# Performance work log

Hardware: AMD Instinct MI355X
Metric: run time of the kernel (lower is better)

Reference implementation:

```python
import jax, jax.numpy as jnp
import numpy as np

HIDDEN_DIM = 256
Z_DIM = 64
B = 8
SRC_LEN = 2048
NUM_DIRS = 2


def setup_inputs() -> dict:
    key = jax.random.key(0)
    ks = jax.random.split(key, 7)
    return {
        "encoder_hidden_state": jax.random.normal(ks[0], (NUM_DIRS, B, HIDDEN_DIM), dtype=jnp.float32),
        "decoder_hidden_state": jax.random.normal(ks[1], (B, HIDDEN_DIM), dtype=jnp.float32),
        "latent_z_seq": jax.random.normal(ks[2], (B, SRC_LEN, Z_DIM), dtype=jnp.float32),
        "mask": jax.random.randint(ks[3], (B, SRC_LEN), 0, 2, dtype=jnp.int32),
        "weight_q": jax.random.normal(ks[4], (HIDDEN_DIM + Z_DIM, HIDDEN_DIM), dtype=jnp.float32),
        "weight_k": jax.random.normal(ks[5], (HIDDEN_DIM + Z_DIM, HIDDEN_DIM), dtype=jnp.float32),
        "weight_v": jax.random.normal(ks[6], (HIDDEN_DIM + Z_DIM, HIDDEN_DIM), dtype=jnp.float32),
    }


def reference(encoder_hidden_state, decoder_hidden_state, latent_z_seq, mask,
              weight_q, weight_k, weight_v):
    # decoder_hidden_state is accepted but unused (as in the original forward).
    src_len = latent_z_seq.shape[1]
    temperature = jnp.asarray(HIDDEN_DIM ** 0.5, latent_z_seq.dtype)
    # sum over directions/layers: [D,B,H] -> [B,H], broadcast along seq
    enc = jnp.sum(encoder_hidden_state, axis=0)  # [B,H]
    enc = jnp.broadcast_to(enc[:, None, :], (enc.shape[0], src_len, enc.shape[1]))
    attn_input = jnp.concatenate((enc, latent_z_seq), axis=2)  # [B,S,H+Z]
    q = jnp.einsum('bsd,dh->bsh', attn_input, weight_q)
    k = jnp.einsum('bsd,dh->bsh', attn_input, weight_k)
    v = jnp.einsum('bsd,dh->bsh', attn_input, weight_v)
    scores = jnp.einsum('bqh,bkh->bqk', q, k) / temperature  # [B,S,S]
    # mask[:, :, None] broadcasts along the key axis (masks query rows)
    scores = jnp.where(mask[:, :, None] == 0, jnp.asarray(-1e9, scores.dtype), scores)
    attn = jax.nn.softmax(scores, axis=-1)
    output = jnp.einsum('bqk,bkh->bqh', attn, v)  # [B,S,H]
    return (output, attn)
```

## Files before the change

### kernel.cpp

```cpp
#include <hip/hip_runtime.h>
#include <hip/hip_bf16.h>

#define B_ 8
#define S_ 2048
#define H_ 256
#define Z_ 64
#define CHK 32
#define NQCH 16
#define BS (B_*S_)

typedef short bf16x8 __attribute__((ext_vector_type(8)));
typedef float f32x4 __attribute__((ext_vector_type(4)));

__device__ __forceinline__ unsigned short f2bf(float f) {
  __hip_bfloat16 h = __float2bfloat16(f);
  return *reinterpret_cast<unsigned short*>(&h);
}
__device__ __forceinline__ float bf2f(unsigned short u) {
  __hip_bfloat16 h;
  *reinterpret_cast<unsigned short*>(&h) = u;
  return __bfloat162float(h);
}
__device__ __forceinline__ unsigned int pack2(float a, float b) {
  return (unsigned int)f2bf(a) | ((unsigned int)f2bf(b) << 16);
}

__device__ __forceinline__ void gl_lds16(const void* g, void* l) {
  __builtin_amdgcn_global_load_lds(
      (const __attribute__((address_space(1))) unsigned int*)(uintptr_t)g,
      (__attribute__((address_space(3))) unsigned int*)(uintptr_t)l,
      16, 0, 0);
}

__global__ __launch_bounds__(256) void k0_base(
    const float* __restrict__ enc, const float* __restrict__ Wq,
    const float* __restrict__ Wk, const float* __restrict__ Wv,
    float* __restrict__ q0, float* __restrict__ k0, float* __restrict__ v0) {
  int b = blockIdx.x;
  int h = threadIdx.x;
  __shared__ float encs[H_];
  encs[h] = enc[b*H_ + h] + enc[B_*H_ + b*H_ + h];
  __syncthreads();
  float aq = 0.f, ak = 0.f, av = 0.f;
  #pragma unroll 4
  for (int d = 0; d < H_; d++) {
    float e = encs[d];
    aq = fmaf(e, Wq[d*H_ + h], aq);
    ak = fmaf(e, Wk[d*H_ + h], ak);
    av = fmaf(e, Wv[d*H_ + h], av);
  }
  q0[b*H_ + h] = aq;
  k0[b*H_ + h] = ak;
  v0[b*H_ + h] = av;
}

__global__ __launch_bounds__(256) void k1_prep(
    const float* __restrict__ z, const float* __restrict__ Wq,
    const float* __restrict__ Wk, const float* __restrict__ Wv,
    const float* __restrict__ q0, const float* __restrict__ k0b, const float* __restrict__ v0,
    unsigned short* __restrict__ Qhi, unsigned short* __restrict__ Qlo,
    unsigned short* __restrict__ Khi, unsigned short* __restrict__ Klo,
    unsigned short* __restrict__ Vt) {
  int b  = blockIdx.x >> 7;
  int st = blockIdx.x & 127;
  int tid = threadIdx.x;
  __shared__ float zs[16*Z_];
  __shared__ float vbuf[16][H_];
  {
    const float4* zp = reinterpret_cast<const float4*>(z + ((size_t)b*S_ + st*16)*Z_);
    reinterpret_cast<float4*>(zs)[tid] = zp[tid];
  }
  __syncthreads();
  float bq = q0[b*H_ + tid], bk = k0b[b*H_ + tid], bv = v0[b*H_ + tid];
  float accq[16], acck[16], accv[16];
  #pragma unroll
  for (int s = 0; s < 16; s++) { accq[s] = bq; acck[s] = bk; accv[s] = bv; }
  #pragma unroll 2
  for (int z0 = 0; z0 < Z_; z0 += 8) {
    float wq[8], wk[8], wv[8];
    #pragma unroll
    for (int j = 0; j < 8; j++) {
      wq[j] = Wq[(H_+z0+j)*H_ + tid];
      wk[j] = Wk[(H_+z0+j)*H_ + tid];
      wv[j] = Wv[(H_+z0+j)*H_ + tid];
    }
    #pragma unroll
    for (int j = 0; j < 8; j++) {
      #pragma unroll
      for (int s = 0; s < 16; s++) {
        float zz = zs[s*Z_ + z0 + j];
        accq[s] = fmaf(zz, wq[j], accq[s]);
        acck[s] = fmaf(zz, wk[j], acck[s]);
        accv[s] = fmaf(zz, wv[j], accv[s]);
      }
    }
  }
  #pragma unroll
  for (int s = 0; s < 16; s++) {
    size_t row = ((size_t)b*S_ + st*16 + s)*H_ + tid;
    unsigned short qh = f2bf(accq[s]);
    Qhi[row] = qh;
    Qlo[row] = f2bf(accq[s] - bf2f(qh));
    unsigned short kh = f2bf(acck[s]);
    Khi[row] = kh;
    Klo[row] = f2bf(acck[s] - bf2f(kh));
    vbuf[s][tid] = accv[s];
  }
  __syncthreads();
  unsigned int pk[8];
  #pragma unroll
  for (int j = 0; j < 8; j++)
    pk[j] = pack2(vbuf[2*j][tid], vbuf[2*j+1][tid]);
  uint4* vt4 = reinterpret_cast<uint4*>(Vt + ((size_t)b*H_ + tid)*S_ + st*16);
  vt4[0] = make_uint4(pk[0], pk[1], pk[2], pk[3]);
  vt4[1] = make_uint4(pk[4], pk[5], pk[6], pk[7]);
}

__global__ __launch_bounds__(256, 2) void k2_flash(
    const unsigned short* __restrict__ Qhi, const unsigned short* __restrict__ Qlo,
    const unsigned short* __restrict__ Khi, const unsigned short* __restrict__ Klo,
    const int* __restrict__ mask,
    float* __restrict__ attn, float* __restrict__ Mq) {
  int bb    = blockIdx.x;
  int b     = bb & 7;
  int strip = (bb >> 3) & 15;
  int kq    = bb >> 7;
  int qb    = strip*128;
  int k0q   = kq*512;
  int tid  = threadIdx.x;
  int wave = tid >> 6;
  int lane = tid & 63;
  int l15  = lane & 15;
  int quad = lane >> 4;
  int qw   = qb + wave*32;

  __shared__ __align__(16) unsigned short KhiL[2][32*256];
  __shared__ __align__(16) unsigned short KloL[2][32*256];

  const unsigned short* KhiB = Khi + (size_t)b*S_*H_;
  const unsigned short* KloB = Klo + (size_t)b*S_*H_;

  int sub = lane >> 5;
  int c5  = lane & 31;

  auto dma_chunk = [&](int c) {
    int buf = c & 1;
    int kc = k0q + c*CHK;
    #pragma unroll
    for (int t = 0; t < 4; t++) {
      int i = wave*4 + t;
      int row = i*2 + sub;
      int lslot = c5 ^ ((row & 15) << 1);
      size_t gs = (size_t)(kc + row)*H_ + lslot*8;
      gl_lds16(KhiB + gs, &KhiL[buf][i*512]);
      gl_lds16(KloB + gs, &KloL[buf][i*512]);
    }
  };

  bf16x8 qh[2][8], ql[2][8];
  #pragma unroll
  for (int qt = 0; qt < 2; qt++) {
    const unsigned short* qhp = Qhi + ((size_t)b*S_ + qw + qt*16 + l15)*H_ + quad*8;
    const unsigned short* qlp = Qlo + ((size_t)b*S_ + qw + qt*16 + l15)*H_ + quad*8;
    #pragma unroll
    for (int dc = 0; dc < 8; dc++) {
      qh[qt][dc] = *reinterpret_cast<const bf16x8*>(qhp + dc*32);
      ql[qt][dc] = *reinterpret_cast<const bf16x8*>(qlp + dc*32);
    }
  }
  int mrow[2][4];
  #pragma unroll
  for (int qt = 0; qt < 2; qt++)
    #pragma unroll
    for (int r = 0; r < 4; r++) mrow[qt][r] = mask[b*S_ + qw + qt*16 + quad*4 + r];

  float m_run[2][4] = {{-1e30f,-1e30f,-1e30f,-1e30f},{-1e30f,-1e30f,-1e30f,-1e30f}};

  dma_chunk(0);
  __syncthreads();

  for (int c = 0; c < NQCH; c++) {
    if (c+1 < NQCH) dma_chunk(c+1);
    int buf = c & 1;
    int kc  = k0q + c*CHK;
    f32x4 sacc[2][2];
    #pragma unroll
    for (int kt = 0; kt < 2; kt++) {
      int row = kt*16 + l15;
      int sw  = (row & 15) << 1;
      const unsigned short* khb = &KhiL[buf][row*256];
      const unsigned short* klb = &KloL[buf][row*256];
      f32x4 a0[2], a1[2];
      #pragma unroll
      for (int qt = 0; qt < 2; qt++) {
        a0[qt] = (f32x4){0.f,0.f,0.f,0.f};
        a1[qt] = (f32x4){0.f,0.f,0.f,0.f};
      }
      #pragma unroll
      for (int dc = 0; dc < 8; dc += 2) {
        int s0 = ((dc*4 + quad) ^ sw) * 8;
        int s1 = (((dc+1)*4 + quad) ^ sw) * 8;
        bf16x8 kh0 = *reinterpret_cast<const bf16x8*>(khb + s0);
        bf16x8 kl0 = *reinterpret_cast<const bf16x8*>(klb + s0);
        bf16x8 kh1 = *reinterpret_cast<const bf16x8*>(khb + s1);
        bf16x8 kl1 = *reinterpret_cast<const bf16x8*>(klb + s1);
        #pragma unroll
        for (int qt = 0; qt < 2; qt++) {
          a0[qt] = __builtin_amdgcn_mfma_f32_16x16x32_bf16(qh[qt][dc],   kh0, a0[qt], 0, 0, 0);
          a1[qt] = __builtin_amdgcn_mfma_f32_16x16x32_bf16(qh[qt][dc+1], kh1, a1[qt], 0, 0, 0);
          a0[qt] = __builtin_amdgcn_mfma_f32_16x16x32_bf16(ql[qt][dc],   kh0, a0[qt], 0, 0, 0);
          a1[qt] = __builtin_amdgcn_mfma_f32_16x16x32_bf16(ql[qt][dc+1], kh1, a1[qt], 0, 0, 0);
          a0[qt] = __builtin_amdgcn_mfma_f32_16x16x32_bf16(qh[qt][dc],   kl0, a0[qt], 0, 0, 0);
          a1[qt] = __builtin_amdgcn_mfma_f32_16x16x32_bf16(qh[qt][dc+1], kl1, a1[qt], 0, 0, 0);
        }
      }
      #pragma unroll
      for (int qt = 0; qt < 2; qt++) sacc[qt][kt] = a0[qt] + a1[qt];
    }
    #pragma unroll
    for (int qt = 0; qt < 2; qt++) {
      #pragma unroll
      for (int r = 0; r < 4; r++) {
        float se0 = mrow[qt][r] ? sacc[qt][0][r]*0.0625f : -1e9f;
        float se1 = mrow[qt][r] ? sacc[qt][1][r]*0.0625f : -1e9f;
        m_run[qt][r] = fmaxf(m_run[qt][r], fmaxf(se0, se1));
        size_t rb = ((size_t)b*S_ + qw + qt*16 + quad*4 + r)*S_ + kc;
        attn[rb + l15]      = se0;
        attn[rb + 16 + l15] = se1;
      }
    }
    __syncthreads();
  }

  #pragma unroll
  for (int qt = 0; qt < 2; qt++) {
    #pragma unroll
    for (int r = 0; r < 4; r++) {
      float m = m_run[qt][r];
      m = fmaxf(m, __shfl_xor(m, 1));
      m = fmaxf(m, __shfl_xor(m, 2));
      m = fmaxf(m, __shfl_xor(m, 4));
      m = fmaxf(m, __shfl_xor(m, 8));
      if (l15 == 0)
        Mq[kq*BS + b*S_ + qw + qt*16 + quad*4 + r] = m;
    }
  }
}

__global__ __launch_bounds__(256) void k3a(
    const float* __restrict__ attn, const unsigned short* __restrict__ Vt,
    const float* __restrict__ Mq, float* __restrict__ outp,
    float* __restrict__ Mfin, float* __restrict__ Lfin) {
  int bb = blockIdx.x;
  int b  = bb & 7;
  int qb = (bb >> 3) * 64;
  int tid  = threadIdx.x;
  int wave = tid >> 6;
  int lane = tid & 63;
  int l15  = lane & 15;
  int quad = lane >> 4;
  int qw   = qb + wave*16;

  __shared__ __align__(16) unsigned short VtL[2][256*64];
  __shared__ float lred[4][16];

  const unsigned short* VtB = Vt + (size_t)b*H_*S_;
  int gr = b*S_ + qw + l15;
  float m = fmaxf(fmaxf(Mq[gr], Mq[BS + gr]), fmaxf(Mq[2*BS + gr], Mq[3*BS + gr]));

  int hsub = lane >> 3;
  int slot = lane & 7;

  auto dma_v = [&](int c) {
    int buf = c & 1;
    int kc = c*64;
    #pragma unroll
    for (int t = 0; t < 8; t++) {
      int i = wave*8 + t;
      int h = i*8 + hsub;
      int lslot = slot ^ (((h >> 2) & 3) << 1);
      gl_lds16(VtB + (size_t)h*S_ + kc + lslot*8, &VtL[buf][i*512]);
    }
  };

  f32x4 acc[16];
  #pragma unroll
  for (int ht = 0; ht < 16; ht++) acc[ht] = (f32x4){0.f, 0.f, 0.f, 0.f};
  float lpart = 0.f;

  const float* sp = attn + (size_t)gr*S_ + quad*8;
  dma_v(0);
  float4 s0 = *reinterpret_cast<const float4*>(sp);
  float4 s1 = *reinterpret_cast<const float4*>(sp + 4);
  float4 s2 = *reinterpret_cast<const float4*>(sp + 32);
  float4 s3 = *reinterpret_cast<const float4*>(sp + 36);
  __syncthreads();

  for (int c = 0; c < 32; c++) {
    if (c+1 < 32) dma_v(c+1);
    int buf = c & 1;
    float4 n0, n1, n2, n3;
    if (c+1 < 32) {
      const float* np = sp + (c+1)*64;
      n0 = *reinterpret_cast<const float4*>(np);
      n1 = *reinterpret_cast<const float4*>(np + 4);
      n2 = *reinterpret_cast<const float4*>(np + 32);
      n3 = *reinterpret_cast<const float4*>(np + 36);
    }
    float p0 = __expf(s0.x - m), p1 = __expf(s0.y - m);
    float p2 = __expf(s0.z - m), p3 = __expf(s0.w - m);
    float p4 = __expf(s1.x - m), p5 = __expf(s1.y - m);
    float p6 = __expf(s1.z - m), p7 = __expf(s1.w - m);
    float q0f = __expf(s2.x - m), q1f = __expf(s2.y - m);
    float q2f = __expf(s2.z - m), q3f = __expf(s2.w - m);
    float q4f = __expf(s3.x - m), q5f = __expf(s3.y - m);
    float q6f = __expf(s3.z - m), q7f = __expf(s3.w - m);
    lpart += p0+p1+p2+p3+p4+p5+p6+p7+q0f+q1f+q2f+q3f+q4f+q5f+q6f+q7f;
    unsigned int pw[4] = {pack2(p0,p1), pack2(p2,p3), pack2(p4,p5), pack2(p6,p7)};
    unsigned int qv[4] = {pack2(q0f,q1f), pack2(q2f,q3f), pack2(q4f,q5f), pack2(q6f,q7f)};
    bf16x8 pa0, pa1;
    memcpy(&pa0, pw, 16);
    memcpy(&pa1, qv, 16);
    int swz = ((l15 >> 2) & 3) << 1;
    #pragma unroll
    for (int ht = 0; ht < 16; ht++) {
      const unsigned short* vb = &VtL[buf][(ht*16 + l15)*64];
      bf16x8 v0 = *reinterpret_cast<const bf16x8*>(vb + (quad ^ swz)*8);
      bf16x8 v1 = *reinterpret_cast<const bf16x8*>(vb + ((4 + quad) ^ swz)*8);
      acc[ht] = __builtin_amdgcn_mfma_f32_16x16x32_bf16(pa0, v0, acc[ht], 0, 0, 0);
      acc[ht] = __builtin_amdgcn_mfma_f32_16x16x32_bf16(pa1, v1, acc[ht], 0, 0, 0);
    }
    s0 = n0; s1 = n1; s2 = n2; s3 = n3;
    __syncthreads();
  }

  lpart += __shfl_xor(lpart, 16);
  lpart += __shfl_xor(lpart, 32);
  if (quad == 0) {
    lred[wave][l15] = lpart;
    Lfin[gr] = lpart;
    Mfin[gr] = m;
  }
  float il[4];
  #pragma unroll
  for (int r = 0; r < 4; r++) il[r] = 1.f / lred[wave][quad*4 + r];
  #pragma unroll
  for (int ht = 0; ht < 16; ht++)
    #pragma unroll
    for (int r = 0; r < 4; r++)
      outp[((size_t)b*S_ + qw + quad*4 + r)*H_ + ht*16 + l15] = acc[ht][r] * il[r];
}

__global__ __launch_bounds__(256) void k3b(
    float* __restrict__ attn, const float* __restrict__ Mfin,
    const float* __restrict__ Lfin) {
  int gr  = blockIdx.x;
  int tid = threadIdx.x;
  float m  = Mfin[gr];
  float il = 1.f / Lfin[gr];
  float4* pa = reinterpret_cast<float4*>(attn + (size_t)gr*S_ + tid*8);
  float4 x0 = pa[0], x1 = pa[1];
  x0.x = __expf(x0.x - m)*il; x0.y = __expf(x0.y - m)*il;
  x0.z = __expf(x0.z - m)*il; x0.w = __expf(x0.w - m)*il;
  x1.x = __expf(x1.x - m)*il; x1.y = __expf(x1.y - m)*il;
  x1.z = __expf(x1.z - m)*il; x1.w = __expf(x1.w - m)*il;
  pa[0] = x0; pa[1] = x1;
}

extern "C" void kernel_launch(void* const* d_in, const int* in_sizes, int n_in,
                              void* d_out, int out_size, void* d_ws, size_t ws_size,
                              hipStream_t stream) {
  const float* enc = (const float*)d_in[0];
  const float* z   = (const float*)d_in[2];
  const int* mask  = (const int*)d_in[3];
  const float* Wq  = (const float*)d_in[4];
  const float* Wk  = (const float*)d_in[5];
  const float* Wv  = (const float*)d_in[6];

  char* ws = (char*)d_ws;
  const size_t MB = 1024*1024;
  unsigned short* Qhi = (unsigned short*)(ws);
  unsigned short* Qlo = (unsigned short*)(ws +  8*MB);
  unsigned short* Khi = (unsigned short*)(ws + 16*MB);
  unsigned short* Klo = (unsigned short*)(ws + 24*MB);
  unsigned short* Vt  = (unsigned short*)(ws + 32*MB);
  float* q0 = (float*)(ws + 40*MB);
  float* k0 = q0 + B_*H_;
  float* v0 = k0 + B_*H_;
  float* Mq   = (float*)(ws + 41*MB);
  float* Mfin = (float*)(ws + 41*MB + 512*1024);
  float* Lfin = (float*)(ws + 41*MB + 512*1024 + 64*1024);

  float* outp = (float*)d_out;
  float* attn = outp + (size_t)B_*S_*H_;

  k0_base<<<B_, 256, 0, stream>>>(enc, Wq, Wk, Wv, q0, k0, v0);
  k1_prep<<<B_*(S_/16), 256, 0, stream>>>(z, Wq, Wk, Wv, q0, k0, v0,
                                          Qhi, Qlo, Khi, Klo, Vt);
  k2_flash<<<B_*(S_/128)*4, 256, 0, stream>>>(Qhi, Qlo, Khi, Klo, mask,
                                              attn, Mq);
  k3a<<<B_*(S_/64), 256, 0, stream>>>(attn, Vt, Mq, outp, Mfin, Lfin);
  k3b<<<B_*S_, 256, 0, stream>>>(attn, Mfin, Lfin);
}
```

Baseline: 338.0 us.

## Compute online softmax denominators in score kernel and fuse normalization into PV kernel

The score kernel now keeps a running row max and an online sum of exponentials for each of its four key quarters and writes both to workspace. The PV kernel merges the four partial (max, sum) pairs up front, normalizes the probabilities before the MFMA, and writes the final attention values back in place. This removes the separate normalization kernel and its full extra read and write of the 128MB attention matrix. In exchange the score loop does more shuffle reductions and exps per chunk.

```diff
diff --git a/kernel.cpp b/kernel.cpp
--- a/kernel.cpp
+++ b/kernel.cpp
@@ -120,7 +120,7 @@
     const unsigned short* __restrict__ Qhi, const unsigned short* __restrict__ Qlo,
     const unsigned short* __restrict__ Khi, const unsigned short* __restrict__ Klo,
     const int* __restrict__ mask,
-    float* __restrict__ attn, float* __restrict__ Mq) {
+    float* __restrict__ attn, float* __restrict__ Mq, float* __restrict__ Lq) {
   int bb    = blockIdx.x;
   int b     = bb & 7;
   int strip = (bb >> 3) & 15;
@@ -175,6 +175,7 @@
     for (int r = 0; r < 4; r++) mrow[qt][r] = mask[b*S_ + qw + qt*16 + quad*4 + r];
 
   float m_run[2][4] = {{-1e30f,-1e30f,-1e30f,-1e30f},{-1e30f,-1e30f,-1e30f,-1e30f}};
+  float l_run[2][4] = {{0.f,0.f,0.f,0.f},{0.f,0.f,0.f,0.f}};
 
   dma_chunk(0);
   __syncthreads();
@@ -223,34 +224,44 @@
       for (int r = 0; r < 4; r++) {
         float se0 = mrow[qt][r] ? sacc[qt][0][r]*0.0625f : -1e9f;
         float se1 = mrow[qt][r] ? sacc[qt][1][r]*0.0625f : -1e9f;
-        m_run[qt][r] = fmaxf(m_run[qt][r], fmaxf(se0, se1));
         size_t rb = ((size_t)b*S_ + qw + qt*16 + quad*4 + r)*S_ + kc;
         attn[rb + l15]      = se0;
         attn[rb + 16 + l15] = se1;
+        float ml = fmaxf(se0, se1);
+        ml = fmaxf(ml, __shfl_xor(ml, 1));
+        ml = fmaxf(ml, __shfl_xor(ml, 2));
+        ml = fmaxf(ml, __shfl_xor(ml, 4));
+        ml = fmaxf(ml, __shfl_xor(ml, 8));
+        float mnew = fmaxf(m_run[qt][r], ml);
+        float alpha = __expf(m_run[qt][r] - mnew);
+        float ls = __expf(se0 - mnew) + __expf(se1 - mnew);
+        ls += __shfl_xor(ls, 1);
+        ls += __shfl_xor(ls, 2);
+        ls += __shfl_xor(ls, 4);
+        ls += __shfl_xor(ls, 8);
+        l_run[qt][r] = l_run[qt][r]*alpha + ls;
+        m_run[qt][r] = mnew;
       }
     }
     __syncthreads();
   }
 
-  #pragma unroll
-  for (int qt = 0; qt < 2; qt++) {
-    #pragma unroll
-    for (int r = 0; r < 4; r++) {
-      float m = m_run[qt][r];
-      m = fmaxf(m, __shfl_xor(m, 1));
-      m = fmaxf(m, __shfl_xor(m, 2));
-      m = fmaxf(m, __shfl_xor(m, 4));
-      m = fmaxf(m, __shfl_xor(m, 8));
-      if (l15 == 0)
-        Mq[kq*BS + b*S_ + qw + qt*16 + quad*4 + r] = m;
-    }
+  if (l15 == 0) {
+    #pragma unroll
+    for (int qt = 0; qt < 2; qt++)
+      #pragma unroll
+      for (int r = 0; r < 4; r++) {
+        int idx = kq*BS + b*S_ + qw + qt*16 + quad*4 + r;
+        Mq[idx] = m_run[qt][r];
+        Lq[idx] = l_run[qt][r];
+      }
   }
 }
 
 __global__ __launch_bounds__(256) void k3a(
-    const float* __restrict__ attn, const unsigned short* __restrict__ Vt,
-    const float* __restrict__ Mq, float* __restrict__ outp,
-    float* __restrict__ Mfin, float* __restrict__ Lfin) {
+    float* __restrict__ attn, const unsigned short* __restrict__ Vt,
+    const float* __restrict__ Mq, const float* __restrict__ Lq,
+    float* __restrict__ outp) {
   int bb = blockIdx.x;
   int b  = bb & 7;
   int qb = (bb >> 3) * 64;
@@ -262,11 +273,14 @@
   int qw   = qb + wave*16;
 
   __shared__ __align__(16) unsigned short VtL[2][256*64];
-  __shared__ float lred[4][16];
 
   const unsigned short* VtB = Vt + (size_t)b*H_*S_;
   int gr = b*S_ + qw + l15;
-  float m = fmaxf(fmaxf(Mq[gr], Mq[BS + gr]), fmaxf(Mq[2*BS + gr], Mq[3*BS + gr]));
+  float m0 = Mq[gr], m1 = Mq[BS+gr], m2 = Mq[2*BS+gr], m3 = Mq[3*BS+gr];
+  float m = fmaxf(fmaxf(m0, m1), fmaxf(m2, m3));
+  float l = Lq[gr]*__expf(m0-m) + Lq[BS+gr]*__expf(m1-m)
+          + Lq[2*BS+gr]*__expf(m2-m) + Lq[3*BS+gr]*__expf(m3-m);
+  float il = 1.f / l;
 
   int hsub = lane >> 3;
   int slot = lane & 7;
@@ -286,9 +300,8 @@
   f32x4 acc[16];
   #pragma unroll
   for (int ht = 0; ht < 16; ht++) acc[ht] = (f32x4){0.f, 0.f, 0.f, 0.f};
-  float lpart = 0.f;
-
-  const float* sp = attn + (size_t)gr*S_ + quad*8;
+
+  float* sp = attn + (size_t)gr*S_ + quad*8;
   dma_v(0);
   float4 s0 = *reinterpret_cast<const float4*>(sp);
   float4 s1 = *reinterpret_cast<const float4*>(sp + 4);
@@ -307,15 +320,19 @@
       n2 = *reinterpret_cast<const float4*>(np + 32);
       n3 = *reinterpret_cast<const float4*>(np + 36);
     }
-    float p0 = __expf(s0.x - m), p1 = __expf(s0.y - m);
-    float p2 = __expf(s0.z - m), p3 = __expf(s0.w - m);
-    float p4 = __expf(s1.x - m), p5 = __expf(s1.y - m);
-    float p6 = __expf(s1.z - m), p7 = __expf(s1.w - m);
-    float q0f = __expf(s2.x - m), q1f = __expf(s2.y - m);
-    float q2f = __expf(s2.z - m), q3f = __expf(s2.w - m);
-    float q4f = __expf(s3.x - m), q5f = __expf(s3.y - m);
-    float q6f = __expf(s3.z - m), q7f = __expf(s3.w - m);
-    lpart += p0+p1+p2+p3+p4+p5+p6+p7+q0f+q1f+q2f+q3f+q4f+q5f+q6f+q7f;
+    float p0 = __expf(s0.x - m)*il, p1 = __expf(s0.y - m)*il;
+    float p2 = __expf(s0.z - m)*il, p3 = __expf(s0.w - m)*il;
+    float p4 = __expf(s1.x - m)*il, p5 = __expf(s1.y - m)*il;
+    float p6 = __expf(s1.z - m)*il, p7 = __expf(s1.w - m)*il;
+    float q0f = __expf(s2.x - m)*il, q1f = __expf(s2.y - m)*il;
+    float q2f = __expf(s2.z - m)*il, q3f = __expf(s2.w - m)*il;
+    float q4f = __expf(s3.x - m)*il, q5f = __expf(s3.y - m)*il;
+    float q6f = __expf(s3.z - m)*il, q7f = __expf(s3.w - m)*il;
+    float* ap = sp + c*64;
+    *reinterpret_cast<float4*>(ap)      = make_float4(p0, p1, p2, p3);
+    *reinterpret_cast<float4*>(ap + 4)  = make_float4(p4, p5, p6, p7);
+    *reinterpret_cast<float4*>(ap + 32) = make_float4(q0f, q1f, q2f, q3f);
+    *reinterpret_cast<float4*>(ap + 36) = make_float4(q4f, q5f, q6f, q7f);
     unsigned int pw[4] = {pack2(p0,p1), pack2(p2,p3), pack2(p4,p5), pack2(p6,p7)};
     unsigned int qv[4] = {pack2(q0f,q1f), pack2(q2f,q3f), pack2(q4f,q5f), pack2(q6f,q7f)};
     bf16x8 pa0, pa1;
@@ -334,37 +351,11 @@
     __syncthreads();
   }
 
-  lpart += __shfl_xor(lpart, 16);
-  lpart += __shfl_xor(lpart, 32);
-  if (quad == 0) {
-    lred[wave][l15] = lpart;
-    Lfin[gr] = lpart;
-    Mfin[gr] = m;
-  }
-  float il[4];
-  #pragma unroll
-  for (int r = 0; r < 4; r++) il[r] = 1.f / lred[wave][quad*4 + r];
   #pragma unroll
   for (int ht = 0; ht < 16; ht++)
     #pragma unroll
     for (int r = 0; r < 4; r++)
-      outp[((size_t)b*S_ + qw + quad*4 + r)*H_ + ht*16 + l15] = acc[ht][r] * il[r];
-}
-
-__global__ __launch_bounds__(256) void k3b(
-    float* __restrict__ attn, const float* __restrict__ Mfin,
-    const float* __restrict__ Lfin) {
-  int gr  = blockIdx.x;
-  int tid = threadIdx.x;
-  float m  = Mfin[gr];
-  float il = 1.f / Lfin[gr];
-  float4* pa = reinterpret_cast<float4*>(attn + (size_t)gr*S_ + tid*8);
-  float4 x0 = pa[0], x1 = pa[1];
-  x0.x = __expf(x0.x - m)*il; x0.y = __expf(x0.y - m)*il;
-  x0.z = __expf(x0.z - m)*il; x0.w = __expf(x0.w - m)*il;
-  x1.x = __expf(x1.x - m)*il; x1.y = __expf(x1.y - m)*il;
-  x1.z = __expf(x1.z - m)*il; x1.w = __expf(x1.w - m)*il;
-  pa[0] = x0; pa[1] = x1;
+      outp[((size_t)b*S_ + qw + quad*4 + r)*H_ + ht*16 + l15] = acc[ht][r];
 }
 
 extern "C" void kernel_launch(void* const* d_in, const int* in_sizes, int n_in,
@@ -387,9 +378,8 @@
   float* q0 = (float*)(ws + 40*MB);
   float* k0 = q0 + B_*H_;
   float* v0 = k0 + B_*H_;
-  float* Mq   = (float*)(ws + 41*MB);
-  float* Mfin = (float*)(ws + 41*MB + 512*1024);
-  float* Lfin = (float*)(ws + 41*MB + 512*1024 + 64*1024);
+  float* Mq = (float*)(ws + 41*MB);
+  float* Lq = (float*)(ws + 41*MB + 512*1024);
 
   float* outp = (float*)d_out;
   float* attn = outp + (size_t)B_*S_*H_;
@@ -398,7 +388,6 @@
   k1_prep<<<B_*(S_/16), 256, 0, stream>>>(z, Wq, Wk, Wv, q0, k0, v0,
                                           Qhi, Qlo, Khi, Klo, Vt);
   k2_flash<<<B_*(S_/128)*4, 256, 0, stream>>>(Qhi, Qlo, Khi, Klo, mask,
-                                              attn, Mq);
-  k3a<<<B_*(S_/64), 256, 0, stream>>>(attn, Vt, Mq, outp, Mfin, Lfin);
-  k3b<<<B_*S_, 256, 0, stream>>>(attn, Mfin, Lfin);
-}
+                                              attn, Mq, Lq);
+  k3a<<<B_*(S_/64), 256, 0, stream>>>(attn, Vt, Mq, Lq, outp);
+}
```

New measurement: 337.9 us. About the same (-0.0%).
